# Kernel optimization log

Hardware: AMD Instinct MI355X
Metric: run time of the kernel (lower is better)

The kernel has to match this reference:

```python
import jax, jax.numpy as jnp
import numpy as np

EPS = 1e-6
NORM_FACTOR = 1000.0  # self.normalization_factor, aggregation 'sum'

# ---- Lorentz manifold (curvature -1, hyperboloid <x,x>_L = -1) ----

def _linner(x, y):
    # Lorentz inner product, keepdim on last axis
    return -x[..., :1] * y[..., :1] + jnp.sum(x[..., 1:] * y[..., 1:], axis=-1, keepdims=True)

def _proj_tan0(u):
    return jnp.concatenate([jnp.zeros_like(u[..., :1]), u[..., 1:]], axis=-1)

def _expmap0(u):
    sp = u[..., 1:]
    n = jnp.sqrt(jnp.clip(jnp.sum(sp * sp, axis=-1, keepdims=True), EPS))
    return jnp.concatenate([jnp.cosh(n), jnp.sinh(n) / n * sp], axis=-1)

def _logmap0(x):
    x0 = jnp.clip(x[..., :1], 1.0 + EPS)
    d = jnp.arccosh(x0)
    sp = x[..., 1:] * (d / jnp.sqrt(x0 * x0 - 1.0))
    return jnp.concatenate([jnp.zeros_like(x0), sp], axis=-1)

def _dist(x, y):
    return jnp.arccosh(jnp.clip(-_linner(x, y), 1.0 + EPS))

def _logmap(x, y):
    alpha = jnp.clip(-_linner(x, y), 1.0 + EPS)
    u = y - alpha * x                      # y + <x,y>_L x
    return jnp.arccosh(alpha) * u / jnp.sqrt(alpha * alpha - 1.0)

def _expmap(x, u):
    n = jnp.sqrt(jnp.clip(_linner(u, u), EPS))
    return jnp.cosh(n) * x + jnp.sinh(n) / n * u

def _proju(x, u):
    return u + _linner(x, u) * x

def _transp0(y, v):
    # parallel transport from origin o=(1,0,...,0) to y
    coef = _linner(y, v) / (1.0 + y[..., :1])
    oy = jnp.concatenate([y[..., :1] + 1.0, y[..., 1:]], axis=-1)
    return v + coef * oy

def _layernorm(x, g, b, eps=1e-5):
    m = jnp.mean(x, axis=-1, keepdims=True)
    v = jnp.mean((x - m) ** 2, axis=-1, keepdims=True)
    return (x - m) / jnp.sqrt(v + eps) * g + b


def setup_inputs() -> dict:
    N, E, D, ED = 10000, 320000, 128, 2
    key = jax.random.key(0)
    ks = jax.random.split(key, 10)
    # nodes on the hyperboloid: expmap0 of a small tangent vector
    h_tan = 0.02 * jax.random.normal(ks[0], (N, D), dtype=jnp.float32)
    h = _expmap0(_proj_tan0(h_tan))
    edge_attr = jax.random.normal(ks[1], (E, ED), dtype=jnp.float32)
    row = jax.random.randint(ks[2], (E,), 0, N, dtype=jnp.int32)
    col = jax.random.randint(ks[3], (E,), 0, N, dtype=jnp.int32)
    node_mask = jnp.ones((N, 1), dtype=jnp.float32)
    edge_mask = jnp.ones((E, 1), dtype=jnp.float32)
    s = 1.0 / np.sqrt(D)
    W = s * jax.random.normal(ks[4], (D, D), dtype=jnp.float32)
    bias = 0.0 * jax.random.normal(ks[5], (1, D), dtype=jnp.float32)  # init.constant_(bias, 0)
    att_in = 2 * D + ED + 1  # x_row, x_col, edge_attr + geodesic
    att_w1 = (1.0 / np.sqrt(att_in)) * jax.random.normal(ks[6], (att_in, D), dtype=jnp.float32)
    att_b1 = jnp.zeros((D,), dtype=jnp.float32)
    att_w2 = s * jax.random.normal(ks[7], (D, 1), dtype=jnp.float32)
    att_b2 = jnp.zeros((1,), dtype=jnp.float32)
    ln_gamma = jnp.ones((D - 1,), dtype=jnp.float32)
    ln_beta = jnp.zeros((D - 1,), dtype=jnp.float32)
    return {"h": h, "edge_attr": edge_attr, "row": row, "col": col,
            "node_mask": node_mask, "edge_mask": edge_mask, "W": W, "bias": bias,
            "att_w1": att_w1, "att_b1": att_b1, "att_w2": att_w2, "att_b2": att_b2,
            "ln_gamma": ln_gamma, "ln_beta": ln_beta}


def reference(h, edge_attr, row, col, node_mask, edge_mask, W, bias,
              att_w1, att_b1, att_w2, att_b2, ln_gamma, ln_beta):
    N = h.shape[0]
    # ---- HypLinear ----
    xt = _logmap0(h) @ W                  # Linear(in,out,bias=False)
    x = _expmap0(_proj_tan0(xt))
    b = _transp0(x, _proj_tan0(bias))
    x = _expmap(x, b)
    # ---- HypAgg ----
    x_tan = _logmap0(x)
    xr, xc = x[row], x[col]
    geo = _dist(xr, xc)                   # [E,1]
    att_in = jnp.concatenate([x_tan[row], x_tan[col], edge_attr, geo], axis=-1)
    hid = jax.nn.silu(att_in @ att_w1 + att_b1)
    att = jax.nn.sigmoid(hid @ att_w2 + att_b2) * edge_mask   # [E,1]
    loc = _logmap(xr, xc)                 # [E,D]
    agg = jax.ops.segment_sum(loc * att, row, num_segments=N) / NORM_FACTOR
    x = _expmap(x, _proju(x, agg))
    # ---- HNorm (Lorentz: LN on spatial components only) ----
    ht = _logmap0(x)
    sp = _layernorm(ht[..., 1:], ln_gamma, ln_beta)
    x = _expmap0(jnp.concatenate([ht[..., :1], sp], axis=-1))
    # ---- HypAct (manifold_out = Lorentz as well) ----
    xt = _proj_tan0(jax.nn.silu(_logmap0(x)))
    return _expmap0(xt)
```

## Files before the change

### kernel.cpp

```cpp
#include <hip/hip_runtime.h>
#include <hip/hip_fp16.h>
#include <math.h>

#define D 128
#define NPB 8
#define EPS1 (1.0f + 1e-6f)

__device__ __forceinline__ float dpp_rsum16(float v) {
    v += __int_as_float(__builtin_amdgcn_update_dpp(
        0, __float_as_int(v), 0x121, 0xf, 0xf, true));
    v += __int_as_float(__builtin_amdgcn_update_dpp(
        0, __float_as_int(v), 0x122, 0xf, 0xf, true));
    v += __int_as_float(__builtin_amdgcn_update_dpp(
        0, __float_as_int(v), 0x124, 0xf, 0xf, true));
    v += __int_as_float(__builtin_amdgcn_update_dpp(
        0, __float_as_int(v), 0x128, 0xf, 0xf, true));
    return v;
}

__device__ __forceinline__ float facosh(float a) {
    return __logf(a + sqrtf(fmaxf(a * a - 1.0f, 0.0f)));
}

__device__ __forceinline__ void unpack8(const float4& a, const float4& b,
                                        float* d) {
    d[0] = a.x; d[1] = a.y; d[2] = a.z; d[3] = a.w;
    d[4] = b.x; d[5] = b.y; d[6] = b.z; d[7] = b.w;
}

__device__ __forceinline__ void unpackh8(const float4& v, float* d) {
    const __half2* p = (const __half2*)&v;
#pragma unroll
    for (int t = 0; t < 4; t++) {
        float2 f = __half22float2(p[t]);
        d[2 * t] = f.x;
        d[2 * t + 1] = f.y;
    }
}

__device__ __forceinline__ void bsumH2(float* v, float (*wred)[2], int lane,
                                       int wid, int kp) {
    __syncthreads();
#pragma unroll
    for (int o = 32; o; o >>= 1)
#pragma unroll
        for (int nl = 0; nl < 2; nl++) v[nl] += __shfl_xor(v[nl], o, 64);
    if (lane == 0)
#pragma unroll
        for (int nl = 0; nl < 2; nl++) wred[wid][nl] = v[nl];
    __syncthreads();
#pragma unroll
    for (int nl = 0; nl < 2; nl++)
        v[nl] = wred[2 * kp][nl] + wred[2 * kp + 1][nl];
}

__global__ __launch_bounds__(512) void node_pre8(
    const float* __restrict__ h, const float* __restrict__ W,
    const float* __restrict__ bias, const float* __restrict__ att_w1,
    const float* __restrict__ att_b1, float* __restrict__ Xrow,
    __half* __restrict__ XQh, float* __restrict__ P_out,
    const int* __restrict__ row, int* __restrict__ cnt, int N, int E) {
    int i0 = blockIdx.x * NPB;
    int tid = threadIdx.x;
    int j = tid & 127, kp = tid >> 7;
    int lane = tid & 63, wid = tid >> 6;
    int nbase = kp * 2;
    __shared__ __align__(16) float t8[NPB][D];
    __shared__ float psumP[4][NPB][D];
    __shared__ float psumQ[4][NPB][D];
    __shared__ float wred[8][2];

    float hj[2];
#pragma unroll
    for (int nl = 0; nl < 2; nl++) {
        int gi = i0 + nbase + nl;
        hj[nl] = (gi < N) ? h[(size_t)gi * D + j] : 0.0f;
        t8[nbase + nl][j] = hj[nl];
    }
    __syncthreads();
    float tj[2];
#pragma unroll
    for (int nl = 0; nl < 2; nl++) {
        float h0 = fmaxf(t8[nbase + nl][0], EPS1);
        float fac = facosh(h0) * rsqrtf(h0 * h0 - 1.0f);
        tj[nl] = (j == 0) ? 0.0f : hj[nl] * fac;
    }
    __syncthreads();
#pragma unroll
    for (int nl = 0; nl < 2; nl++) t8[nbase + nl][j] = tj[nl];
    __syncthreads();

    float xtp[NPB];
#pragma unroll
    for (int n = 0; n < NPB; n++) xtp[n] = 0.0f;
    int kbeg = kp * 32;
    for (int k0 = kbeg; k0 < kbeg + 32; k0 += 4) {
        float w0 = W[(k0 + 0) * D + j], w1 = W[(k0 + 1) * D + j];
        float w2 = W[(k0 + 2) * D + j], w3 = W[(k0 + 3) * D + j];
#pragma unroll
        for (int n = 0; n < NPB; n++) {
            float4 tv = *(const float4*)&t8[n][k0];
            xtp[n] = fmaf(tv.x, w0,
                          fmaf(tv.y, w1, fmaf(tv.z, w2, fmaf(tv.w, w3, xtp[n]))));
        }
    }
#pragma unroll
    for (int n = 0; n < NPB; n++) psumP[kp][n][j] = xtp[n];
    __syncthreads();
    float xt[2];
#pragma unroll
    for (int nl = 0; nl < 2; nl++) {
        int n = nbase + nl;
        xt[nl] = (j == 0) ? 0.0f
                          : (psumP[0][n][j] + psumP[1][n][j] + psumP[2][n][j] +
                             psumP[3][n][j]);
    }

    float v2[2];
#pragma unroll
    for (int nl = 0; nl < 2; nl++) v2[nl] = xt[nl] * xt[nl];
    bsumH2(v2, wred, lane, wid, kp);
    float xj[2];
#pragma unroll
    for (int nl = 0; nl < 2; nl++) {
        float nn = sqrtf(fmaxf(v2[nl], 1e-6f));
        float e = __expf(nn), ei = __fdividef(1.0f, e);
        float ch = 0.5f * (e + ei), sh = 0.5f * (e - ei);
        xj[nl] = (j == 0) ? ch : __fdividef(sh, nn) * xt[nl];
    }

    float vj = (j == 0) ? 0.0f : bias[j];
#pragma unroll
    for (int nl = 0; nl < 2; nl++) v2[nl] = xj[nl] * vj;
    bsumH2(v2, wred, lane, wid, kp);
    __syncthreads();
#pragma unroll
    for (int nl = 0; nl < 2; nl++) t8[nbase + nl][j] = xj[nl];
    __syncthreads();
    float bj[2];
#pragma unroll
    for (int nl = 0; nl < 2; nl++) {
        float X0 = t8[nbase + nl][0];
        float coef = __fdividef(v2[nl], 1.0f + X0);
        bj[nl] = vj + coef * ((j == 0) ? (X0 + 1.0f) : xj[nl]);
    }
#pragma unroll
    for (int nl = 0; nl < 2; nl++)
        v2[nl] = (j == 0) ? -bj[nl] * bj[nl] : bj[nl] * bj[nl];
    bsumH2(v2, wred, lane, wid, kp);
    float xnj[2];
#pragma unroll
    for (int nl = 0; nl < 2; nl++) {
        float nb = sqrtf(fmaxf(v2[nl], 1e-6f));
        float e = __expf(nb), ei = __fdividef(1.0f, e);
        float ch = 0.5f * (e + ei), sh = 0.5f * (e - ei);
        xnj[nl] = ch * xj[nl] + __fdividef(sh, nb) * bj[nl];
        int gi = i0 + nbase + nl;
        if (gi < N) {
            Xrow[(size_t)gi * D + j] = xnj[nl];
            XQh[(size_t)gi * 256 + j] = __float2half(xnj[nl]);
        }
    }

    __syncthreads();
#pragma unroll
    for (int nl = 0; nl < 2; nl++) t8[nbase + nl][j] = xnj[nl];
    __syncthreads();
    float xtj[2];
#pragma unroll
    for (int nl = 0; nl < 2; nl++) {
        float Y0 = fmaxf(t8[nbase + nl][0], EPS1);
        float f = facosh(Y0) * rsqrtf(Y0 * Y0 - 1.0f);
        xtj[nl] = (j == 0) ? 0.0f : xnj[nl] * f;
    }
    __syncthreads();
#pragma unroll
    for (int nl = 0; nl < 2; nl++) t8[nbase + nl][j] = xtj[nl];
    __syncthreads();

    float pp[NPB], qq[NPB];
#pragma unroll
    for (int n = 0; n < NPB; n++) {
        pp[n] = 0.0f;
        qq[n] = 0.0f;
    }
    for (int k0 = kbeg; k0 < kbeg + 32; k0 += 4) {
        float a0 = att_w1[(k0 + 0) * D + j], a1 = att_w1[(k0 + 1) * D + j];
        float a2 = att_w1[(k0 + 2) * D + j], a3 = att_w1[(k0 + 3) * D + j];
        float c0 = att_w1[(D + k0 + 0) * D + j], c1 = att_w1[(D + k0 + 1) * D + j];
        float c2 = att_w1[(D + k0 + 2) * D + j], c3 = att_w1[(D + k0 + 3) * D + j];
#pragma unroll
        for (int n = 0; n < NPB; n++) {
            float4 tv = *(const float4*)&t8[n][k0];
            pp[n] = fmaf(tv.x, a0,
                         fmaf(tv.y, a1, fmaf(tv.z, a2, fmaf(tv.w, a3, pp[n]))));
            qq[n] = fmaf(tv.x, c0,
                         fmaf(tv.y, c1, fmaf(tv.z, c2, fmaf(tv.w, c3, qq[n]))));
        }
    }
#pragma unroll
    for (int n = 0; n < NPB; n++) {
        psumP[kp][n][j] = pp[n];
        psumQ[kp][n][j] = qq[n];
    }
    __syncthreads();
    float b1 = att_b1[j];
#pragma unroll
    for (int nl = 0; nl < 2; nl++) {
        int n = nbase + nl;
        int gi = i0 + n;
        if (gi < N) {
            P_out[(size_t)gi * D + j] = psumP[0][n][j] + psumP[1][n][j] +
                                        psumP[2][n][j] + psumP[3][n][j] + b1;
            float q = psumQ[0][n][j] + psumQ[1][n][j] + psumQ[2][n][j] +
                      psumQ[3][n][j];
            XQh[(size_t)gi * 256 + 128 + j] = __float2half(q);
        }
    }

    int gtid = blockIdx.x * 512 + tid;
    int tot = gridDim.x * 512;
    for (int e2 = gtid; e2 < E; e2 += tot) atomicAdd(&cnt[row[e2]], 1);
}

__global__ __launch_bounds__(1024) void scan_kernel(const int* __restrict__ cnt,
                                                    int* __restrict__ off,
                                                    int* __restrict__ cursor,
                                                    int N) {
    __shared__ int wt[16];
    int tid = threadIdx.x, lane = tid & 63, wid = tid >> 6;
    int PER = (N + 1023) >> 10;
    int basei = tid * PER;
    int loc[16];
    int tsum = 0;
#pragma unroll 4
    for (int r = 0; r < PER; r++) {
        int idx = basei + r;
        int v = (idx < N) ? cnt[idx] : 0;
        loc[r] = tsum;
        tsum += v;
    }
    int inc = tsum;
#pragma unroll
    for (int o = 1; o < 64; o <<= 1) {
        int t = __shfl_up(inc, o, 64);
        if (lane >= o) inc += t;
    }
    if (lane == 63) wt[wid] = inc;
    __syncthreads();
    if (tid < 16) {
        int w = wt[tid];
#pragma unroll
        for (int o = 1; o < 16; o <<= 1) {
            int t = __shfl_up(w, o, 64);
            if ((tid & 15) >= o) w += t;
        }
        wt[tid] = w;
    }
    __syncthreads();
    int wbase = (wid == 0) ? 0 : wt[wid - 1];
    int texcl = wbase + inc - tsum;
    for (int r = 0; r < PER; r++) {
        int idx = basei + r;
        if (idx < N) {
            int o = texcl + loc[r];
            off[idx] = o;
            cursor[idx] = o;
        }
    }
}

__global__ void scatter_kernel(const int* __restrict__ row,
                               const int* __restrict__ col,
                               const float* __restrict__ edge_attr,
                               const float* __restrict__ edge_mask,
                               int* __restrict__ cursor,
                               float4* __restrict__ rec, int E) {
    const float2* ea2 = (const float2*)edge_attr;
    for (int e = blockIdx.x * blockDim.x + threadIdx.x; e < E;
         e += gridDim.x * blockDim.x) {
        int r = row[e];
        int pos = atomicAdd(&cursor[r], 1);
        float2 a = ea2[e];
        rec[pos] = make_float4(__int_as_float(col[e]), a.x, a.y, edge_mask[e]);
    }
}

__global__ __launch_bounds__(256) void edge_agg(
    const float* __restrict__ Xrow, const float* __restrict__ P,
    const __half* __restrict__ XQh, const float4* __restrict__ rec,
    const int* __restrict__ off, const int* __restrict__ cnt,
    const float* __restrict__ w1c, const float* __restrict__ att_w2,
    const float* __restrict__ att_b2, float* __restrict__ aggP, int N) {
    int tid = threadIdx.x, lane = tid & 63, wid = tid >> 6;
    int sub = lane & 15, grp = lane >> 4, gb = lane & 48;
    int i = blockIdx.x * 2 + (wid >> 1);
    int w = wid & 1;
    bool valid = i < N;
    i = min(i, N - 1);
    int f4 = sub * 2;

    const float4* w4 = (const float4*)w1c;
    const float4* aw4 = (const float4*)att_w2;
    const float4* xr4 = (const float4*)(Xrow + (size_t)i * D);
    const float4* pr4 = (const float4*)(P + (size_t)i * D);
    float xr[8], pr[8], wa[8], wb[8], wg[8], w2v[8];
    unpack8(xr4[f4], xr4[f4 + 1], xr);
    unpack8(pr4[f4], pr4[f4 + 1], pr);
    unpack8(w4[f4], w4[f4 + 1], wa);
    unpack8(w4[32 + f4], w4[32 + f4 + 1], wb);
    unpack8(w4[64 + f4], w4[64 + f4 + 1], wg);
    unpack8(aw4[f4], aw4[f4 + 1], w2v);
    float b2 = att_b2[0];
    float xr0s = (sub == 0) ? -xr[0] : xr[0];

    float acc[8];
#pragma unroll
    for (int u = 0; u < 8; u++) acc[u] = 0.0f;

    int s = off[i], m = valid ? cnt[i] : 0;
    int clen = (m + 7) >> 3;
    int base = (w * 4 + grp) * clen;
    int len = min(m - base, clen);
    if (len < 0) len = 0;

    float4 rp = make_float4(__int_as_float(0), 0.0f, 0.0f, 0.0f);
    if (sub < len) rp = rec[s + base + sub];
    int colp = __float_as_int(rp.x);

    auto computeE = [&](float eay, float eaz, float msk, bool act,
                        const float4& g0, const float4& g1) {
        float xc[8], qc[8];
        unpackh8(g0, xc);
        unpackh8(g1, qc);
        float lin = xr0s * xc[0];
#pragma unroll
        for (int u = 1; u < 8; u++) lin = fmaf(xr[u], xc[u], lin);
        lin = dpp_rsum16(lin);
        float alpha = fmaxf(-lin, EPS1);
        float a2m = fmaxf(fmaf(alpha, alpha, -1.0f), 1e-12f);
        float rden = rsqrtf(a2m);
        float geo = __logf(fmaf(a2m, rden, alpha));
        float lp = 0.0f;
#pragma unroll
        for (int u = 0; u < 8; u++) {
            float hv = pr[u] + qc[u] +
                       fmaf(eay, wa[u], fmaf(eaz, wb[u], geo * wg[u]));
            float sig = __fdividef(1.0f, 1.0f + __expf(-hv));
            lp = fmaf(hv * sig, w2v[u], lp);
        }
        lp = dpp_rsum16(lp);
        float wq = act ? msk : 0.0f;
        float att = wq * __fdividef(1.0f, 1.0f + __expf(-(lp + b2)));
        float scale = att * geo * rden * 1e-3f;
#pragma unroll
        for (int u = 0; u < 8; u++)
            acc[u] = fmaf(scale, fmaf(-alpha, xr[u], xc[u]), acc[u]);
    };

    int tmax = min(clen, 16);

    {
        int c0 = __shfl(colp, gb | 0, 64);
        const float4* p0 = (const float4*)(XQh + (size_t)c0 * 256);
        float4 gA0 = p0[sub], gA1 = p0[16 + sub];
        int c1 = __shfl(colp, gb | 1, 64);
        const float4* p1 = (const float4*)(XQh + (size_t)c1 * 256);
        float4 gB0 = p1[sub], gB1 = p1[16 + sub];
        float4 gC0, gC1;

        for (int t = 0; t < tmax; ++t) {
            int cn = __shfl(colp, gb | ((t + 2) & 15), 64);
            const float4* pn = (const float4*)(XQh + (size_t)cn * 256);
            gC0 = pn[sub];
            gC1 = pn[16 + sub];
            float eay = __shfl(rp.y, gb | t, 64);
            float eaz = __shfl(rp.z, gb | t, 64);
            float msk = __shfl(rp.w, gb | t, 64);
            computeE(eay, eaz, msk, t < len, gA0, gA1);
            gA0 = gB0; gA1 = gB1;
            gB0 = gC0; gB1 = gC1;
        }
    }
    for (int t = 16; t < clen; ++t) {
        bool act = t < len;
        float4 rc = make_float4(__int_as_float(0), 0.0f, 0.0f, 0.0f);
        if (act) rc = rec[s + base + t];
        const float4* pt =
            (const float4*)(XQh + (size_t)__float_as_int(rc.x) * 256);
        float4 g0 = pt[sub], g1 = pt[16 + sub];
        computeE(rc.y, rc.z, rc.w, act, g0, g1);
    }

#pragma unroll
    for (int u = 0; u < 8; u++) {
        acc[u] += __shfl_xor(acc[u], 16, 64);
        acc[u] += __shfl_xor(acc[u], 32, 64);
    }
    if (valid && grp == 0) {
        float4* a4 = (float4*)(aggP + (size_t)(2 * i + w) * D);
        a4[f4] = make_float4(acc[0], acc[1], acc[2], acc[3]);
        a4[f4 + 1] = make_float4(acc[4], acc[5], acc[6], acc[7]);
    }
}

__global__ __launch_bounds__(256) void node_post(
    const float* __restrict__ Xrow, const float* __restrict__ aggP,
    const float* __restrict__ gamma, const float* __restrict__ beta,
    float* __restrict__ out, int N) {
    int tid = threadIdx.x, lane = tid & 63;
    int sub = lane & 15;
    int i = blockIdx.x * 16 + (tid >> 4);
    bool valid = i < N;
    i = min(i, N - 1);
    int j8 = sub * 8, f4 = sub * 2;

    const float4* xr4 = (const float4*)(Xrow + (size_t)i * D);
    const float4* a4a = (const float4*)(aggP + (size_t)(2 * i) * D);
    const float4* a4b = (const float4*)(aggP + (size_t)(2 * i + 1) * D);
    float xr[8], p0[8], p1[8], acc[8];
    unpack8(xr4[f4], xr4[f4 + 1], xr);
    unpack8(a4a[f4], a4a[f4 + 1], p0);
    unpack8(a4b[f4], a4b[f4 + 1], p1);
#pragma unroll
    for (int u = 0; u < 8; u++) acc[u] = p0[u] + p1[u];

    float lxa_p = (sub == 0) ? -xr[0] * acc[0] : xr[0] * acc[0];
#pragma unroll
    for (int u = 1; u < 8; u++) lxa_p = fmaf(xr[u], acc[u], lxa_p);
    float lxa = dpp_rsum16(lxa_p);
    float uj[8];
#pragma unroll
    for (int u = 0; u < 8; u++) uj[u] = fmaf(lxa, xr[u], acc[u]);
    float luu_p = (sub == 0) ? -uj[0] * uj[0] : uj[0] * uj[0];
#pragma unroll
    for (int u = 1; u < 8; u++) luu_p = fmaf(uj[u], uj[u], luu_p);
    float luu = dpp_rsum16(luu_p);
    float nn = sqrtf(fmaxf(luu, 1e-6f));
    float e = __expf(nn), ei = __fdividef(1.0f, e);
    float ch = 0.5f * (e + ei), shv = __fdividef(0.5f * (e - ei), nn);
    float xn[8];
#pragma unroll
    for (int u = 0; u < 8; u++) xn[u] = ch * xr[u] + shv * uj[u];
    float X0 = __shfl(xn[0], lane & 48, 64);
    X0 = fmaxf(X0, EPS1);
    float fc = facosh(X0) * rsqrtf(X0 * X0 - 1.0f);
    float ht[8];
#pragma unroll
    for (int u = 0; u < 8; u++) ht[u] = xn[u] * fc;
    if (sub == 0) ht[0] = 0.0f;
    float mp = 0.0f;
#pragma unroll
    for (int u = 0; u < 8; u++) mp += ht[u];
    float mean = dpp_rsum16(mp) * (1.0f / 127.0f);
    float diff[8];
#pragma unroll
    for (int u = 0; u < 8; u++) diff[u] = ht[u] - mean;
    if (sub == 0) diff[0] = 0.0f;
    float vp = 0.0f;
#pragma unroll
    for (int u = 0; u < 8; u++) vp = fmaf(diff[u], diff[u], vp);
    float var = dpp_rsum16(vp) * (1.0f / 127.0f);
    float rstd = rsqrtf(var + 1e-5f);
    float sp[8];
#pragma unroll
    for (int u = 0; u < 8; u++) {
        int j = j8 + u;
        float g = (j > 0) ? gamma[j - 1] : 0.0f;
        float bt = (j > 0) ? beta[j - 1] : 0.0f;
        sp[u] = fmaf(diff[u] * rstd, g, bt);
    }
    if (sub == 0) sp[0] = 0.0f;
    float n2p = 0.0f;
#pragma unroll
    for (int u = 0; u < 8; u++) n2p = fmaf(sp[u], sp[u], n2p);
    float n2 = sqrtf(fmaxf(dpp_rsum16(n2p), 1e-6f));
    e = __expf(n2);
    ei = __fdividef(1.0f, e);
    float y0 = 0.5f * (e + ei), sh2 = __fdividef(0.5f * (e - ei), n2);
    float yj[8];
#pragma unroll
    for (int u = 0; u < 8; u++) yj[u] = sh2 * sp[u];
    if (sub == 0) yj[0] = y0;
    float y0c = fmaxf(y0, EPS1);
    float f3 = facosh(y0c) * rsqrtf(y0c * y0c - 1.0f);
    float sj[8];
#pragma unroll
    for (int u = 0; u < 8; u++) {
        float lj = yj[u] * f3;
        sj[u] = __fdividef(lj, 1.0f + __expf(-lj));
    }
    if (sub == 0) sj[0] = 0.0f;
    float n3p = 0.0f;
#pragma unroll
    for (int u = 0; u < 8; u++) n3p = fmaf(sj[u], sj[u], n3p);
    float n3 = sqrtf(fmaxf(dpp_rsum16(n3p), 1e-6f));
    e = __expf(n3);
    ei = __fdividef(1.0f, e);
    float o0 = 0.5f * (e + ei), sh3 = __fdividef(0.5f * (e - ei), n3);
    float ov[8];
#pragma unroll
    for (int u = 0; u < 8; u++) ov[u] = sh3 * sj[u];
    if (sub == 0) ov[0] = o0;
    if (valid) {
        float4* o4 = (float4*)(out + (size_t)i * D);
        o4[f4] = make_float4(ov[0], ov[1], ov[2], ov[3]);
        o4[f4 + 1] = make_float4(ov[4], ov[5], ov[6], ov[7]);
    }
}

extern "C" void kernel_launch(void* const* d_in, const int* in_sizes, int n_in,
                              void* d_out, int out_size, void* d_ws,
                              size_t ws_size, hipStream_t stream) {
    const float* h = (const float*)d_in[0];
    const float* edge_attr = (const float*)d_in[1];
    const int* row = (const int*)d_in[2];
    const int* col = (const int*)d_in[3];
    const float* edge_mask = (const float*)d_in[5];
    const float* W = (const float*)d_in[6];
    const float* bias = (const float*)d_in[7];
    const float* att_w1 = (const float*)d_in[8];
    const float* att_b1 = (const float*)d_in[9];
    const float* att_w2 = (const float*)d_in[10];
    const float* att_b2 = (const float*)d_in[11];
    const float* ln_g = (const float*)d_in[12];
    const float* ln_b = (const float*)d_in[13];

    int N = in_sizes[0] / D;
    int E = in_sizes[2];

    float* Xrow = (float*)d_ws;
    float* Pbuf = Xrow + (size_t)N * D;
    __half* XQh = (__half*)(Pbuf + (size_t)N * D);
    float4* rec = (float4*)(XQh + (size_t)N * 256);
    int* cnt = (int*)(rec + E);
    int* off = cnt + N;
    int* cur = off + N;
    float* aggP = (float*)(cur + N);

    hipMemsetAsync(cnt, 0, N * sizeof(int), stream);
    node_pre8<<<(N + NPB - 1) / NPB, 512, 0, stream>>>(
        h, W, bias, att_w1, att_b1, Xrow, XQh, Pbuf, row, cnt, N, E);
    scan_kernel<<<1, 1024, 0, stream>>>(cnt, off, cur, N);
    scatter_kernel<<<640, 256, 0, stream>>>(row, col, edge_attr, edge_mask,
                                            cur, rec, E);
    edge_agg<<<(N + 1) / 2, 256, 0, stream>>>(Xrow, Pbuf, XQh, rec, off, cnt,
                                              att_w1 + 256 * D, att_w2,
                                              att_b2, aggP, N);
    node_post<<<(N + 15) / 16, 256, 0, stream>>>(Xrow, aggP, ln_g, ln_b,
                                                 (float*)d_out, N);
}
```

Before: 146.4 us.

## Move edge scatter into node pre-kernel and use per-wave node reductions

The row-count histogram becomes its own kernel that runs before the scan. The edge scatter into CSR records is folded into the tail of node_pre8, which now runs after the scan. Inside node_pre8 each of the 8 waves owns one node with two elements per lane, so the per-node norm reductions use in-wave DPP and shuffles instead of the block-wide shared-memory reductions and their many barriers. Launch count stays the same, but the scatter now shares a kernel with the matmul-heavy node work, which could lengthen that kernel's tail.

```diff
diff --git a/kernel.cpp b/kernel.cpp
--- a/kernel.cpp
+++ b/kernel.cpp
@@ -3,7 +3,6 @@
 #include <math.h>
 
 #define D 128
-#define NPB 8
 #define EPS1 (1.0f + 1e-6f)
 
 __device__ __forceinline__ float dpp_rsum16(float v) {
@@ -18,6 +17,13 @@
     return v;
 }
 
+__device__ __forceinline__ float wsum64(float v) {
+    v = dpp_rsum16(v);
+    v += __shfl_xor(v, 16, 64);
+    v += __shfl_xor(v, 32, 64);
+    return v;
+}
+
 __device__ __forceinline__ float facosh(float a) {
     return __logf(a + sqrtf(fmaxf(a * a - 1.0f, 0.0f)));
 }
@@ -38,189 +44,11 @@
     }
 }
 
-__device__ __forceinline__ void bsumH2(float* v, float (*wred)[2], int lane,
-                                       int wid, int kp) {
-    __syncthreads();
-#pragma unroll
-    for (int o = 32; o; o >>= 1)
-#pragma unroll
-        for (int nl = 0; nl < 2; nl++) v[nl] += __shfl_xor(v[nl], o, 64);
-    if (lane == 0)
-#pragma unroll
-        for (int nl = 0; nl < 2; nl++) wred[wid][nl] = v[nl];
-    __syncthreads();
-#pragma unroll
-    for (int nl = 0; nl < 2; nl++)
-        v[nl] = wred[2 * kp][nl] + wred[2 * kp + 1][nl];
-}
-
-__global__ __launch_bounds__(512) void node_pre8(
-    const float* __restrict__ h, const float* __restrict__ W,
-    const float* __restrict__ bias, const float* __restrict__ att_w1,
-    const float* __restrict__ att_b1, float* __restrict__ Xrow,
-    __half* __restrict__ XQh, float* __restrict__ P_out,
-    const int* __restrict__ row, int* __restrict__ cnt, int N, int E) {
-    int i0 = blockIdx.x * NPB;
-    int tid = threadIdx.x;
-    int j = tid & 127, kp = tid >> 7;
-    int lane = tid & 63, wid = tid >> 6;
-    int nbase = kp * 2;
-    __shared__ __align__(16) float t8[NPB][D];
-    __shared__ float psumP[4][NPB][D];
-    __shared__ float psumQ[4][NPB][D];
-    __shared__ float wred[8][2];
-
-    float hj[2];
-#pragma unroll
-    for (int nl = 0; nl < 2; nl++) {
-        int gi = i0 + nbase + nl;
-        hj[nl] = (gi < N) ? h[(size_t)gi * D + j] : 0.0f;
-        t8[nbase + nl][j] = hj[nl];
-    }
-    __syncthreads();
-    float tj[2];
-#pragma unroll
-    for (int nl = 0; nl < 2; nl++) {
-        float h0 = fmaxf(t8[nbase + nl][0], EPS1);
-        float fac = facosh(h0) * rsqrtf(h0 * h0 - 1.0f);
-        tj[nl] = (j == 0) ? 0.0f : hj[nl] * fac;
-    }
-    __syncthreads();
-#pragma unroll
-    for (int nl = 0; nl < 2; nl++) t8[nbase + nl][j] = tj[nl];
-    __syncthreads();
-
-    float xtp[NPB];
-#pragma unroll
-    for (int n = 0; n < NPB; n++) xtp[n] = 0.0f;
-    int kbeg = kp * 32;
-    for (int k0 = kbeg; k0 < kbeg + 32; k0 += 4) {
-        float w0 = W[(k0 + 0) * D + j], w1 = W[(k0 + 1) * D + j];
-        float w2 = W[(k0 + 2) * D + j], w3 = W[(k0 + 3) * D + j];
-#pragma unroll
-        for (int n = 0; n < NPB; n++) {
-            float4 tv = *(const float4*)&t8[n][k0];
-            xtp[n] = fmaf(tv.x, w0,
-                          fmaf(tv.y, w1, fmaf(tv.z, w2, fmaf(tv.w, w3, xtp[n]))));
-        }
-    }
-#pragma unroll
-    for (int n = 0; n < NPB; n++) psumP[kp][n][j] = xtp[n];
-    __syncthreads();
-    float xt[2];
-#pragma unroll
-    for (int nl = 0; nl < 2; nl++) {
-        int n = nbase + nl;
-        xt[nl] = (j == 0) ? 0.0f
-                          : (psumP[0][n][j] + psumP[1][n][j] + psumP[2][n][j] +
-                             psumP[3][n][j]);
-    }
-
-    float v2[2];
-#pragma unroll
-    for (int nl = 0; nl < 2; nl++) v2[nl] = xt[nl] * xt[nl];
-    bsumH2(v2, wred, lane, wid, kp);
-    float xj[2];
-#pragma unroll
-    for (int nl = 0; nl < 2; nl++) {
-        float nn = sqrtf(fmaxf(v2[nl], 1e-6f));
-        float e = __expf(nn), ei = __fdividef(1.0f, e);
-        float ch = 0.5f * (e + ei), sh = 0.5f * (e - ei);
-        xj[nl] = (j == 0) ? ch : __fdividef(sh, nn) * xt[nl];
-    }
-
-    float vj = (j == 0) ? 0.0f : bias[j];
-#pragma unroll
-    for (int nl = 0; nl < 2; nl++) v2[nl] = xj[nl] * vj;
-    bsumH2(v2, wred, lane, wid, kp);
-    __syncthreads();
-#pragma unroll
-    for (int nl = 0; nl < 2; nl++) t8[nbase + nl][j] = xj[nl];
-    __syncthreads();
-    float bj[2];
-#pragma unroll
-    for (int nl = 0; nl < 2; nl++) {
-        float X0 = t8[nbase + nl][0];
-        float coef = __fdividef(v2[nl], 1.0f + X0);
-        bj[nl] = vj + coef * ((j == 0) ? (X0 + 1.0f) : xj[nl]);
-    }
-#pragma unroll
-    for (int nl = 0; nl < 2; nl++)
-        v2[nl] = (j == 0) ? -bj[nl] * bj[nl] : bj[nl] * bj[nl];
-    bsumH2(v2, wred, lane, wid, kp);
-    float xnj[2];
-#pragma unroll
-    for (int nl = 0; nl < 2; nl++) {
-        float nb = sqrtf(fmaxf(v2[nl], 1e-6f));
-        float e = __expf(nb), ei = __fdividef(1.0f, e);
-        float ch = 0.5f * (e + ei), sh = 0.5f * (e - ei);
-        xnj[nl] = ch * xj[nl] + __fdividef(sh, nb) * bj[nl];
-        int gi = i0 + nbase + nl;
-        if (gi < N) {
-            Xrow[(size_t)gi * D + j] = xnj[nl];
-            XQh[(size_t)gi * 256 + j] = __float2half(xnj[nl]);
-        }
-    }
-
-    __syncthreads();
-#pragma unroll
-    for (int nl = 0; nl < 2; nl++) t8[nbase + nl][j] = xnj[nl];
-    __syncthreads();
-    float xtj[2];
-#pragma unroll
-    for (int nl = 0; nl < 2; nl++) {
-        float Y0 = fmaxf(t8[nbase + nl][0], EPS1);
-        float f = facosh(Y0) * rsqrtf(Y0 * Y0 - 1.0f);
-        xtj[nl] = (j == 0) ? 0.0f : xnj[nl] * f;
-    }
-    __syncthreads();
-#pragma unroll
-    for (int nl = 0; nl < 2; nl++) t8[nbase + nl][j] = xtj[nl];
-    __syncthreads();
-
-    float pp[NPB], qq[NPB];
-#pragma unroll
-    for (int n = 0; n < NPB; n++) {
-        pp[n] = 0.0f;
-        qq[n] = 0.0f;
-    }
-    for (int k0 = kbeg; k0 < kbeg + 32; k0 += 4) {
-        float a0 = att_w1[(k0 + 0) * D + j], a1 = att_w1[(k0 + 1) * D + j];
-        float a2 = att_w1[(k0 + 2) * D + j], a3 = att_w1[(k0 + 3) * D + j];
-        float c0 = att_w1[(D + k0 + 0) * D + j], c1 = att_w1[(D + k0 + 1) * D + j];
-        float c2 = att_w1[(D + k0 + 2) * D + j], c3 = att_w1[(D + k0 + 3) * D + j];
-#pragma unroll
-        for (int n = 0; n < NPB; n++) {
-            float4 tv = *(const float4*)&t8[n][k0];
-            pp[n] = fmaf(tv.x, a0,
-                         fmaf(tv.y, a1, fmaf(tv.z, a2, fmaf(tv.w, a3, pp[n]))));
-            qq[n] = fmaf(tv.x, c0,
-                         fmaf(tv.y, c1, fmaf(tv.z, c2, fmaf(tv.w, c3, qq[n]))));
-        }
-    }
-#pragma unroll
-    for (int n = 0; n < NPB; n++) {
-        psumP[kp][n][j] = pp[n];
-        psumQ[kp][n][j] = qq[n];
-    }
-    __syncthreads();
-    float b1 = att_b1[j];
-#pragma unroll
-    for (int nl = 0; nl < 2; nl++) {
-        int n = nbase + nl;
-        int gi = i0 + n;
-        if (gi < N) {
-            P_out[(size_t)gi * D + j] = psumP[0][n][j] + psumP[1][n][j] +
-                                        psumP[2][n][j] + psumP[3][n][j] + b1;
-            float q = psumQ[0][n][j] + psumQ[1][n][j] + psumQ[2][n][j] +
-                      psumQ[3][n][j];
-            XQh[(size_t)gi * 256 + 128 + j] = __float2half(q);
-        }
-    }
-
-    int gtid = blockIdx.x * 512 + tid;
-    int tot = gridDim.x * 512;
-    for (int e2 = gtid; e2 < E; e2 += tot) atomicAdd(&cnt[row[e2]], 1);
+__global__ void hist_kernel(const int* __restrict__ row, int* __restrict__ cnt,
+                            int E) {
+    for (int e = blockIdx.x * blockDim.x + threadIdx.x; e < E;
+         e += gridDim.x * blockDim.x)
+        atomicAdd(&cnt[row[e]], 1);
 }
 
 __global__ __launch_bounds__(1024) void scan_kernel(const int* __restrict__ cnt,
@@ -270,15 +98,154 @@
     }
 }
 
-__global__ void scatter_kernel(const int* __restrict__ row,
-                               const int* __restrict__ col,
-                               const float* __restrict__ edge_attr,
-                               const float* __restrict__ edge_mask,
-                               int* __restrict__ cursor,
-                               float4* __restrict__ rec, int E) {
+__global__ __launch_bounds__(512) void node_pre8(
+    const float* __restrict__ h, const float* __restrict__ W,
+    const float* __restrict__ bias, const float* __restrict__ att_w1,
+    const float* __restrict__ att_b1, float* __restrict__ Xrow,
+    __half* __restrict__ XQh, float* __restrict__ P_out,
+    const int* __restrict__ row, const int* __restrict__ col,
+    const float* __restrict__ edge_attr, const float* __restrict__ edge_mask,
+    int* __restrict__ cursor, float4* __restrict__ rec, int N, int E) {
+    int i0 = blockIdx.x * 8;
+    int tid = threadIdx.x;
+    int j = tid & 127, kp = tid >> 7;
+    int lane = tid & 63, wv = tid >> 6;
+    int j0 = 2 * lane;
+    __shared__ __align__(16) float t8[8][D];
+    __shared__ float psP[4][8][D];
+    __shared__ float psQ[4][8][D];
+
+    bool vA = (i0 + wv) < N;
+    size_t gA = min(i0 + wv, N - 1);
+
+    float2 hA = *(const float2*)&h[gA * D + j0];
+    float h0A = fmaxf(__shfl(hA.x, 0, 64), EPS1);
+    float facA = facosh(h0A) * rsqrtf(h0A * h0A - 1.0f);
+    float tax = (lane == 0) ? 0.0f : hA.x * facA;
+    float tay = hA.y * facA;
+    *(float2*)&t8[wv][j0] = make_float2(tax, tay);
+    __syncthreads();
+
+    {
+        float xtp[8];
+#pragma unroll
+        for (int n = 0; n < 8; n++) xtp[n] = 0.0f;
+        int kbeg = kp * 32;
+        for (int k0 = kbeg; k0 < kbeg + 32; k0 += 4) {
+            float w0 = W[(k0 + 0) * D + j], w1 = W[(k0 + 1) * D + j];
+            float w2 = W[(k0 + 2) * D + j], w3 = W[(k0 + 3) * D + j];
+#pragma unroll
+            for (int n = 0; n < 8; n++) {
+                float4 tv = *(const float4*)&t8[n][k0];
+                xtp[n] = fmaf(
+                    tv.x, w0,
+                    fmaf(tv.y, w1, fmaf(tv.z, w2, fmaf(tv.w, w3, xtp[n]))));
+            }
+        }
+#pragma unroll
+        for (int n = 0; n < 8; n++) psP[kp][n][j] = xtp[n];
+    }
+    __syncthreads();
+
+    float xnax, xnay;
+    {
+        float2 a0 = *(const float2*)&psP[0][wv][j0];
+        float2 a1 = *(const float2*)&psP[1][wv][j0];
+        float2 a2 = *(const float2*)&psP[2][wv][j0];
+        float2 a3 = *(const float2*)&psP[3][wv][j0];
+        float xtax = a0.x + a1.x + a2.x + a3.x;
+        float xtay = a0.y + a1.y + a2.y + a3.y;
+        if (lane == 0) xtax = 0.0f;
+
+        float nsqA = wsum64(xtax * xtax + xtay * xtay);
+        float nnA = sqrtf(fmaxf(nsqA, 1e-6f));
+        float eA = __expf(nnA), eiA = __fdividef(1.0f, eA);
+        float chA = 0.5f * (eA + eiA), shA = __fdividef(0.5f * (eA - eiA), nnA);
+        float xax = (lane == 0) ? chA : shA * xtax;
+        float xay = shA * xtay;
+
+        float2 bv = *(const float2*)&bias[j0];
+        float va = (lane == 0) ? 0.0f : bv.x, vb = bv.y;
+        float lxvA = wsum64(xax * va + xay * vb);
+        float coefA = __fdividef(lxvA, 1.0f + chA);
+        float baA = (lane == 0) ? coefA * (chA + 1.0f) : fmaf(coefA, xax, va);
+        float bbA = fmaf(coefA, xay, vb);
+        float lbbA = wsum64(((lane == 0) ? -baA * baA : baA * baA) + bbA * bbA);
+        float nbA = sqrtf(fmaxf(lbbA, 1e-6f));
+        float e2A = __expf(nbA), ei2A = __fdividef(1.0f, e2A);
+        float ch2A = 0.5f * (e2A + ei2A);
+        float sh2A = __fdividef(0.5f * (e2A - ei2A), nbA);
+        xnax = ch2A * xax + sh2A * baA;
+        xnay = ch2A * xay + sh2A * bbA;
+        if (vA) {
+            *(float2*)&Xrow[gA * D + j0] = make_float2(xnax, xnay);
+            *(__half2*)&XQh[gA * 256 + j0] =
+                __float22half2_rn(make_float2(xnax, xnay));
+        }
+
+        float Y0A = fmaxf(__shfl(xnax, 0, 64), EPS1);
+        float fA = facosh(Y0A) * rsqrtf(Y0A * Y0A - 1.0f);
+        float x2ax = (lane == 0) ? 0.0f : xnax * fA;
+        float x2ay = xnay * fA;
+        *(float2*)&t8[wv][j0] = make_float2(x2ax, x2ay);
+    }
+    __syncthreads();
+
+    {
+        float pp[8], qq[8];
+#pragma unroll
+        for (int n = 0; n < 8; n++) {
+            pp[n] = 0.0f;
+            qq[n] = 0.0f;
+        }
+        int kbeg = kp * 32;
+        for (int k0 = kbeg; k0 < kbeg + 32; k0 += 4) {
+            float a0 = att_w1[(k0 + 0) * D + j], a1 = att_w1[(k0 + 1) * D + j];
+            float a2 = att_w1[(k0 + 2) * D + j], a3 = att_w1[(k0 + 3) * D + j];
+            float c0 = att_w1[(D + k0 + 0) * D + j];
+            float c1 = att_w1[(D + k0 + 1) * D + j];
+            float c2 = att_w1[(D + k0 + 2) * D + j];
+            float c3 = att_w1[(D + k0 + 3) * D + j];
+#pragma unroll
+            for (int n = 0; n < 8; n++) {
+                float4 tv = *(const float4*)&t8[n][k0];
+                pp[n] = fmaf(
+                    tv.x, a0,
+                    fmaf(tv.y, a1, fmaf(tv.z, a2, fmaf(tv.w, a3, pp[n]))));
+                qq[n] = fmaf(
+                    tv.x, c0,
+                    fmaf(tv.y, c1, fmaf(tv.z, c2, fmaf(tv.w, c3, qq[n]))));
+            }
+        }
+#pragma unroll
+        for (int n = 0; n < 8; n++) {
+            psP[kp][n][j] = pp[n];
+            psQ[kp][n][j] = qq[n];
+        }
+    }
+    __syncthreads();
+
+    if (vA) {
+        float2 b1v = *(const float2*)&att_b1[j0];
+        float2 a0 = *(const float2*)&psP[0][wv][j0];
+        float2 a1 = *(const float2*)&psP[1][wv][j0];
+        float2 a2 = *(const float2*)&psP[2][wv][j0];
+        float2 a3 = *(const float2*)&psP[3][wv][j0];
+        float2 q0 = *(const float2*)&psQ[0][wv][j0];
+        float2 q1 = *(const float2*)&psQ[1][wv][j0];
+        float2 q2 = *(const float2*)&psQ[2][wv][j0];
+        float2 q3 = *(const float2*)&psQ[3][wv][j0];
+        *(float2*)&P_out[gA * D + j0] =
+            make_float2(a0.x + a1.x + a2.x + a3.x + b1v.x,
+                        a0.y + a1.y + a2.y + a3.y + b1v.y);
+        *(__half2*)&XQh[gA * 256 + 128 + j0] = __float22half2_rn(
+            make_float2(q0.x + q1.x + q2.x + q3.x, q0.y + q1.y + q2.y + q3.y));
+    }
+
     const float2* ea2 = (const float2*)edge_attr;
-    for (int e = blockIdx.x * blockDim.x + threadIdx.x; e < E;
-         e += gridDim.x * blockDim.x) {
+    int gtid = blockIdx.x * 512 + tid;
+    int tot = gridDim.x * 512;
+    for (int e = gtid; e < E; e += tot) {
         int r = row[e];
         int pos = atomicAdd(&cursor[r], 1);
         float2 a = ea2[e];
@@ -359,7 +326,6 @@
     };
 
     int tmax = min(clen, 16);
-
     {
         int c0 = __shfl(colp, gb | 0, 64);
         const float4* p0 = (const float4*)(XQh + (size_t)c0 * 256);
@@ -465,9 +431,9 @@
     float sp[8];
 #pragma unroll
     for (int u = 0; u < 8; u++) {
-        int j = j8 + u;
-        float g = (j > 0) ? gamma[j - 1] : 0.0f;
-        float bt = (j > 0) ? beta[j - 1] : 0.0f;
+        int jj = j8 + u;
+        float g = (jj > 0) ? gamma[jj - 1] : 0.0f;
+        float bt = (jj > 0) ? beta[jj - 1] : 0.0f;
         sp[u] = fmaf(diff[u] * rstd, g, bt);
     }
     if (sub == 0) sp[0] = 0.0f;
@@ -539,11 +505,11 @@
     float* aggP = (float*)(cur + N);
 
     hipMemsetAsync(cnt, 0, N * sizeof(int), stream);
-    node_pre8<<<(N + NPB - 1) / NPB, 512, 0, stream>>>(
-        h, W, bias, att_w1, att_b1, Xrow, XQh, Pbuf, row, cnt, N, E);
+    hist_kernel<<<640, 256, 0, stream>>>(row, cnt, E);
     scan_kernel<<<1, 1024, 0, stream>>>(cnt, off, cur, N);
-    scatter_kernel<<<640, 256, 0, stream>>>(row, col, edge_attr, edge_mask,
-                                            cur, rec, E);
+    node_pre8<<<(N + 7) / 8, 512, 0, stream>>>(
+        h, W, bias, att_w1, att_b1, Xrow, XQh, Pbuf, row, col, edge_attr,
+        edge_mask, cur, rec, N, E);
     edge_agg<<<(N + 1) / 2, 256, 0, stream>>>(Xrow, Pbuf, XQh, rec, off, cnt,
                                               att_w1 + 256 * D, att_w2,
                                               att_b2, aggP, N);
```

Measured after the change: 140.2 us. 1.04x faster.
